# Kernel optimization log

Measured on AMD Instinct MI355X. Metric: run time of the kernel, lower is better.

The kernel has to match this reference:

```python
import jax, jax.numpy as jnp
import numpy as np

B = 16384
F_IN = 768
F_OUT = 512

def setup_inputs() -> dict:
    key = jax.random.key(0)
    k1, k2, k3, k4, k5, k6 = jax.random.split(key, 6)
    # densified sparse multi-hot boards (post to_dense())
    stm = jax.random.uniform(k1, (B, F_IN), dtype=jnp.float32)
    nstm = jax.random.uniform(k2, (B, F_IN), dtype=jnp.float32)
    s1 = 1.0 / np.sqrt(F_IN)
    s2 = 1.0 / np.sqrt(2 * F_OUT)
    W1 = jax.random.normal(k3, (F_OUT, F_IN), dtype=jnp.float32) * s1
    b1 = jax.random.normal(k4, (F_OUT,), dtype=jnp.float32) * s1
    W2 = jax.random.normal(k5, (1, 2 * F_OUT), dtype=jnp.float32) * s2
    b2 = jax.random.normal(k6, (1,), dtype=jnp.float32) * s2
    return {"stm": stm, "nstm": nstm, "W1": W1, "b1": b1, "W2": W2, "b2": b2}

def reference(stm, nstm, W1, b1, W2, b2):
    # shared feature transformer applied to both perspectives
    stm_p = stm @ W1.T + b1    # [B, F_OUT]
    nstm_p = nstm @ W1.T + b1  # [B, F_OUT]
    hidden = jnp.clip(jnp.concatenate((stm_p, nstm_p), axis=1), 0.0, 1.0)  # [B, 2*F_OUT]
    return jax.nn.sigmoid(hidden @ W2.T + b2)  # [B, 1]
```

## Files before the change

### kernel.cpp

```cpp
#include <hip/hip_runtime.h>
#include <hip/hip_bf16.h>

#define BATCH 16384
#define FIN   768
#define FOUT  512

#define BK 64
#define NT (FIN / BK)
#define BM 128
#define BN 256

typedef __attribute__((ext_vector_type(8))) short short8;
typedef __attribute__((ext_vector_type(4))) float floatx4;

__device__ __forceinline__ unsigned int cvt_pk_bf16(float a, float b) {
    unsigned int r;
    asm("v_cvt_pk_bf16_f32 %0, %1, %2" : "=v"(r) : "v"(a), "v"(b));
    return r;
}

__device__ __forceinline__ void load_lds_16(const void* g, void* l) {
    __builtin_amdgcn_global_load_lds(
        (const __attribute__((address_space(1))) unsigned int*)g,
        (__attribute__((address_space(3))) unsigned int*)l,
        16, 0, 0);
}

__global__ __launch_bounds__(256) void cvt_w1(
    const float* __restrict__ W1, unsigned short* __restrict__ W1b)
{
    int base = (blockIdx.x * 256 + threadIdx.x) * 8;
    float4 a = *(const float4*)(W1 + base);
    float4 b = *(const float4*)(W1 + base + 4);
    uint4 o;
    o.x = cvt_pk_bf16(a.x, a.y); o.y = cvt_pk_bf16(a.z, a.w);
    o.z = cvt_pk_bf16(b.x, b.y); o.w = cvt_pk_bf16(b.z, b.w);
    *(uint4*)(W1b + base) = o;
}

__global__ __launch_bounds__(512, 2) void pn_gemm(
    const float* __restrict__ stm, const float* __restrict__ nstm,
    const unsigned short* __restrict__ W1b, const float* __restrict__ b1,
    const float* __restrict__ W2, float* __restrict__ P)
{
    __shared__ __align__(16) unsigned short As[2][256 * 64];
    __shared__ __align__(16) unsigned short Bs[2][256 * 64];

    const int tid  = threadIdx.x;
    const int lane = tid & 63;
    const int wave = tid >> 6;
    const int wr   = wave >> 2;
    const int wc   = wave & 3;
    const int quad = lane >> 4;
    const int l16  = lane & 15;

    const int sbid  = (blockIdx.x & 7) * 32 + (blockIdx.x >> 3);
    const int bm    = sbid >> 1;
    const int n_idx = sbid & 1;
    const int b0    = bm * BM;
    const int n0    = n_idx * BN;

    const int arow = tid >> 1;
    const int h    = tid & 1;
    const float* aSrc =
        ((arow < BM) ? stm  + (size_t)(b0 + arow) * FIN
                     : nstm + (size_t)(b0 + arow - BM) * FIN) + h * 32;
    int aOff[4];
    #pragma unroll
    for (int c = 0; c < 4; ++c)
        aOff[c] = arow * 64 + (((h * 4 + c) ^ (arow & 7)) * 8);

    const int brow = lane >> 3;
    const int bch  = (lane & 7) ^ brow;
    const unsigned short* bSrc =
        W1b + (size_t)(n0 + brow) * FIN + bch * 8;

    floatx4 acc[8][4];
    #pragma unroll
    for (int i = 0; i < 8; ++i)
        #pragma unroll
        for (int j = 0; j < 4; ++j)
            acc[i][j] = (floatx4)0.0f;

    float4 ap[8];
    #pragma unroll
    for (int c = 0; c < 4; ++c) {
        ap[2 * c]     = *(const float4*)(aSrc + c * 8);
        ap[2 * c + 1] = *(const float4*)(aSrc + c * 8 + 4);
    }
    #pragma unroll
    for (int i = 0; i < 4; ++i) {
        const int J = wave * 4 + i;
        load_lds_16(bSrc + (size_t)(J * 8) * FIN, &Bs[0][J * 512]);
    }

    for (int t = 0; t < NT; ++t) {
        const int cur = t & 1;
        const int nxt = cur ^ 1;

        #pragma unroll
        for (int c = 0; c < 4; ++c) {
            uint4 o;
            o.x = cvt_pk_bf16(ap[2 * c].x, ap[2 * c].y);
            o.y = cvt_pk_bf16(ap[2 * c].z, ap[2 * c].w);
            o.z = cvt_pk_bf16(ap[2 * c + 1].x, ap[2 * c + 1].y);
            o.w = cvt_pk_bf16(ap[2 * c + 1].z, ap[2 * c + 1].w);
            *(uint4*)(&As[cur][aOff[c]]) = o;
        }
        __syncthreads();

        if (t + 1 < NT) {
            const int kn = (t + 1) * BK;
            #pragma unroll
            for (int c = 0; c < 4; ++c) {
                ap[2 * c]     = *(const float4*)(aSrc + kn + c * 8);
                ap[2 * c + 1] = *(const float4*)(aSrc + kn + c * 8 + 4);
            }
            #pragma unroll
            for (int i = 0; i < 4; ++i) {
                const int J = wave * 4 + i;
                load_lds_16(bSrc + (size_t)(J * 8) * FIN + kn, &Bs[nxt][J * 512]);
            }
        }

        #pragma unroll
        for (int kk = 0; kk < 2; ++kk) {
            const int c = kk * 4 + quad;
            short8 af[8], bfr[4];
            #pragma unroll
            for (int mi = 0; mi < 8; ++mi) {
                const int m = wr * 128 + mi * 16 + l16;
                af[mi] = *(const short8*)(&As[cur][m * 64 + ((c ^ (m & 7)) * 8)]);
            }
            #pragma unroll
            for (int ni = 0; ni < 4; ++ni) {
                const int n = wc * 64 + ni * 16 + l16;
                bfr[ni] = *(const short8*)(&Bs[cur][n * 64 + ((c ^ (n & 7)) * 8)]);
            }
            __builtin_amdgcn_s_setprio(1);
            #pragma unroll
            for (int mi = 0; mi < 8; ++mi)
                #pragma unroll
                for (int ni = 0; ni < 4; ++ni)
                    acc[mi][ni] = __builtin_amdgcn_mfma_f32_16x16x32_bf16(
                        af[mi], bfr[ni], acc[mi][ni], 0, 0, 0);
            __builtin_amdgcn_s_setprio(0);
        }
    }

    float b1v[4], w2v[4];
    const float* w2base = (wr == 0) ? W2 : W2 + FOUT;
    #pragma unroll
    for (int ni = 0; ni < 4; ++ni) {
        int col = n0 + wc * 64 + ni * 16 + l16;
        b1v[ni] = b1[col];
        w2v[ni] = w2base[col];
    }

    __syncthreads();
    float* Epi = (float*)As;

    #pragma unroll
    for (int mi = 0; mi < 8; ++mi) {
        #pragma unroll
        for (int r = 0; r < 4; ++r) {
            float s = 0.0f;
            #pragma unroll
            for (int ni = 0; ni < 4; ++ni) {
                float hh = acc[mi][ni][r] + b1v[ni];
                hh = fminf(fmaxf(hh, 0.0f), 1.0f);
                s += hh * w2v[ni];
            }
            s += __shfl_xor(s, 1);
            s += __shfl_xor(s, 2);
            s += __shfl_xor(s, 4);
            s += __shfl_xor(s, 8);
            if (l16 == 0) {
                Epi[(wr * 128 + mi * 16 + quad * 4 + r) * 4 + wc] = s;
            }
        }
    }
    __syncthreads();

    if (tid < BM) {
        float x = 0.0f;
        #pragma unroll
        for (int j = 0; j < 4; ++j)
            x += Epi[tid * 4 + j] + Epi[(tid + BM) * 4 + j];
        P[n_idx * BATCH + b0 + tid] = x;
    }
}

__global__ __launch_bounds__(256) void finish(
    const float* __restrict__ P, const float* __restrict__ b2,
    float* __restrict__ out)
{
    int i = blockIdx.x * 256 + threadIdx.x;
    float x = b2[0] + P[i] + P[BATCH + i];
    out[i] = 1.0f / (1.0f + expf(-x));
}

extern "C" void kernel_launch(void* const* d_in, const int* in_sizes, int n_in,
                              void* d_out, int out_size, void* d_ws, size_t ws_size,
                              hipStream_t stream)
{
    (void)in_sizes; (void)n_in; (void)out_size; (void)ws_size;
    const float* stm  = (const float*)d_in[0];
    const float* nstm = (const float*)d_in[1];
    const float* W1   = (const float*)d_in[2];
    const float* b1   = (const float*)d_in[3];
    const float* W2   = (const float*)d_in[4];
    const float* b2   = (const float*)d_in[5];
    float* out = (float*)d_out;
    unsigned short* W1b = (unsigned short*)d_ws;
    float* P = (float*)((char*)d_ws + FOUT * FIN * 2);

    cvt_w1<<<dim3((FOUT * FIN) / (256 * 8)), dim3(256), 0, stream>>>(W1, W1b);
    pn_gemm<<<dim3((BATCH / BM) * 2), dim3(512), 0, stream>>>(
        stm, nstm, W1b, b1, W2, P);
    finish<<<dim3(BATCH / 256), dim3(256), 0, stream>>>(P, b2, out);
}
```

Baseline: 163.7 us.

## Split GEMM k-step into four barrier-fenced MFMA phases with triple-buffered B

The main loop is restructured into four sub-phases, each handling half the M fragments and half the K chunk. Each phase is fenced by explicit s_barrier and sched_barrier so LDS fragment reads, the async global→LDS copies of W1 and the bf16 conversion of the next A tile are interleaved between MFMA bursts. B moves to a three-slot ring, prefetched two tiles ahead, and the A conversion and store for the next tile move to the end of the iteration. The goal is to hide global and LDS latency behind MFMA work. The cost is more barriers per tile and LDS growing to the full 160KB per block, and correctness depends on implicit vmcnt ordering for the async B loads.

```diff
diff --git a/kernel.cpp b/kernel.cpp
--- a/kernel.cpp
+++ b/kernel.cpp
@@ -25,6 +25,18 @@
         (__attribute__((address_space(3))) unsigned int*)l,
         16, 0, 0);
 }
+
+#define PH_OPEN() do {                                               \
+    __builtin_amdgcn_sched_barrier(0);                               \
+    __builtin_amdgcn_s_barrier();                                    \
+    asm volatile("s_waitcnt lgkmcnt(0)" ::: "memory");               \
+    __builtin_amdgcn_sched_barrier(0);                               \
+} while (0)
+#define PH_CLOSE() do {                                              \
+    __builtin_amdgcn_sched_barrier(0);                               \
+    __builtin_amdgcn_s_barrier();                                    \
+    __builtin_amdgcn_sched_barrier(0);                               \
+} while (0)
 
 __global__ __launch_bounds__(256) void cvt_w1(
     const float* __restrict__ W1, unsigned short* __restrict__ W1b)
@@ -44,7 +56,7 @@
     const float* __restrict__ W2, float* __restrict__ P)
 {
     __shared__ __align__(16) unsigned short As[2][256 * 64];
-    __shared__ __align__(16) unsigned short Bs[2][256 * 64];
+    __shared__ __align__(16) unsigned short Bs[3][256 * 64];
 
     const int tid  = threadIdx.x;
     const int lane = tid & 63;
@@ -82,6 +94,16 @@
         for (int j = 0; j < 4; ++j)
             acc[i][j] = (floatx4)0.0f;
 
+    #pragma unroll
+    for (int i = 0; i < 4; ++i) {
+        const int J = wave * 4 + i;
+        load_lds_16(bSrc + (size_t)(J * 8) * FIN, &Bs[0][J * 512]);
+    }
+    #pragma unroll
+    for (int i = 0; i < 4; ++i) {
+        const int J = wave * 4 + i;
+        load_lds_16(bSrc + (size_t)(J * 8) * FIN + BK, &Bs[1][J * 512]);
+    }
     float4 ap[8];
     #pragma unroll
     for (int c = 0; c < 4; ++c) {
@@ -89,25 +111,24 @@
         ap[2 * c + 1] = *(const float4*)(aSrc + c * 8 + 4);
     }
     #pragma unroll
-    for (int i = 0; i < 4; ++i) {
-        const int J = wave * 4 + i;
-        load_lds_16(bSrc + (size_t)(J * 8) * FIN, &Bs[0][J * 512]);
-    }
-
+    for (int c = 0; c < 4; ++c) {
+        uint4 o;
+        o.x = cvt_pk_bf16(ap[2 * c].x, ap[2 * c].y);
+        o.y = cvt_pk_bf16(ap[2 * c].z, ap[2 * c].w);
+        o.z = cvt_pk_bf16(ap[2 * c + 1].x, ap[2 * c + 1].y);
+        o.w = cvt_pk_bf16(ap[2 * c + 1].z, ap[2 * c + 1].w);
+        *(uint4*)(&As[0][aOff[c]]) = o;
+    }
+    __builtin_amdgcn_sched_barrier(0);
+    asm volatile("s_waitcnt lgkmcnt(0)" ::: "memory");
+    __builtin_amdgcn_s_barrier();
+    __builtin_amdgcn_sched_barrier(0);
+
+    int bc = 0;
     for (int t = 0; t < NT; ++t) {
         const int cur = t & 1;
-        const int nxt = cur ^ 1;
-
-        #pragma unroll
-        for (int c = 0; c < 4; ++c) {
-            uint4 o;
-            o.x = cvt_pk_bf16(ap[2 * c].x, ap[2 * c].y);
-            o.y = cvt_pk_bf16(ap[2 * c].z, ap[2 * c].w);
-            o.z = cvt_pk_bf16(ap[2 * c + 1].x, ap[2 * c + 1].y);
-            o.w = cvt_pk_bf16(ap[2 * c + 1].z, ap[2 * c + 1].w);
-            *(uint4*)(&As[cur][aOff[c]]) = o;
-        }
-        __syncthreads();
+        int bp = bc + 2; if (bp >= 3) bp -= 3;
+        short8 af[4], bf0[4], bf1[4];
 
         if (t + 1 < NT) {
             const int kn = (t + 1) * BK;
@@ -116,36 +137,122 @@
                 ap[2 * c]     = *(const float4*)(aSrc + kn + c * 8);
                 ap[2 * c + 1] = *(const float4*)(aSrc + kn + c * 8 + 4);
             }
-            #pragma unroll
-            for (int i = 0; i < 4; ++i) {
-                const int J = wave * 4 + i;
-                load_lds_16(bSrc + (size_t)(J * 8) * FIN + kn, &Bs[nxt][J * 512]);
-            }
-        }
-
-        #pragma unroll
-        for (int kk = 0; kk < 2; ++kk) {
-            const int c = kk * 4 + quad;
-            short8 af[8], bfr[4];
-            #pragma unroll
-            for (int mi = 0; mi < 8; ++mi) {
-                const int m = wr * 128 + mi * 16 + l16;
-                af[mi] = *(const short8*)(&As[cur][m * 64 + ((c ^ (m & 7)) * 8)]);
-            }
+        }
+        {
+            const int c0 = quad;
             #pragma unroll
             for (int ni = 0; ni < 4; ++ni) {
                 const int n = wc * 64 + ni * 16 + l16;
-                bfr[ni] = *(const short8*)(&Bs[cur][n * 64 + ((c ^ (n & 7)) * 8)]);
-            }
-            __builtin_amdgcn_s_setprio(1);
-            #pragma unroll
-            for (int mi = 0; mi < 8; ++mi)
-                #pragma unroll
-                for (int ni = 0; ni < 4; ++ni)
-                    acc[mi][ni] = __builtin_amdgcn_mfma_f32_16x16x32_bf16(
-                        af[mi], bfr[ni], acc[mi][ni], 0, 0, 0);
-            __builtin_amdgcn_s_setprio(0);
-        }
+                bf0[ni] = *(const short8*)(&Bs[bc][n * 64 + ((c0 ^ (n & 7)) * 8)]);
+            }
+            #pragma unroll
+            for (int mi = 0; mi < 4; ++mi) {
+                const int m = wr * 128 + mi * 16 + l16;
+                af[mi] = *(const short8*)(&As[cur][m * 64 + ((c0 ^ (m & 7)) * 8)]);
+            }
+        }
+        PH_OPEN();
+        __builtin_amdgcn_s_setprio(1);
+        #pragma unroll
+        for (int mi = 0; mi < 4; ++mi)
+            #pragma unroll
+            for (int ni = 0; ni < 4; ++ni)
+                acc[mi][ni] = __builtin_amdgcn_mfma_f32_16x16x32_bf16(
+                    af[mi], bf0[ni], acc[mi][ni], 0, 0, 0);
+        __builtin_amdgcn_s_setprio(0);
+        PH_CLOSE();
+
+        if (t + 2 < NT) {
+            const size_t kn2 = (size_t)(t + 2) * BK;
+            #pragma unroll
+            for (int i = 0; i < 2; ++i) {
+                const int J = wave * 4 + i;
+                load_lds_16(bSrc + (size_t)(J * 8) * FIN + kn2, &Bs[bp][J * 512]);
+            }
+        }
+        {
+            const int c0 = quad;
+            #pragma unroll
+            for (int mi = 0; mi < 4; ++mi) {
+                const int m = wr * 128 + (mi + 4) * 16 + l16;
+                af[mi] = *(const short8*)(&As[cur][m * 64 + ((c0 ^ (m & 7)) * 8)]);
+            }
+        }
+        PH_OPEN();
+        __builtin_amdgcn_s_setprio(1);
+        #pragma unroll
+        for (int mi = 0; mi < 4; ++mi)
+            #pragma unroll
+            for (int ni = 0; ni < 4; ++ni)
+                acc[mi + 4][ni] = __builtin_amdgcn_mfma_f32_16x16x32_bf16(
+                    af[mi], bf0[ni], acc[mi + 4][ni], 0, 0, 0);
+        __builtin_amdgcn_s_setprio(0);
+        PH_CLOSE();
+
+        if (t + 2 < NT) {
+            const size_t kn2 = (size_t)(t + 2) * BK;
+            #pragma unroll
+            for (int i = 2; i < 4; ++i) {
+                const int J = wave * 4 + i;
+                load_lds_16(bSrc + (size_t)(J * 8) * FIN + kn2, &Bs[bp][J * 512]);
+            }
+        }
+        {
+            const int c1 = 4 + quad;
+            #pragma unroll
+            for (int ni = 0; ni < 4; ++ni) {
+                const int n = wc * 64 + ni * 16 + l16;
+                bf1[ni] = *(const short8*)(&Bs[bc][n * 64 + ((c1 ^ (n & 7)) * 8)]);
+            }
+            #pragma unroll
+            for (int mi = 0; mi < 4; ++mi) {
+                const int m = wr * 128 + mi * 16 + l16;
+                af[mi] = *(const short8*)(&As[cur][m * 64 + ((c1 ^ (m & 7)) * 8)]);
+            }
+        }
+        PH_OPEN();
+        __builtin_amdgcn_s_setprio(1);
+        #pragma unroll
+        for (int mi = 0; mi < 4; ++mi)
+            #pragma unroll
+            for (int ni = 0; ni < 4; ++ni)
+                acc[mi][ni] = __builtin_amdgcn_mfma_f32_16x16x32_bf16(
+                    af[mi], bf1[ni], acc[mi][ni], 0, 0, 0);
+        __builtin_amdgcn_s_setprio(0);
+        PH_CLOSE();
+
+        if (t + 1 < NT) {
+            const int nxt = cur ^ 1;
+            #pragma unroll
+            for (int c = 0; c < 4; ++c) {
+                uint4 o;
+                o.x = cvt_pk_bf16(ap[2 * c].x, ap[2 * c].y);
+                o.y = cvt_pk_bf16(ap[2 * c].z, ap[2 * c].w);
+                o.z = cvt_pk_bf16(ap[2 * c + 1].x, ap[2 * c + 1].y);
+                o.w = cvt_pk_bf16(ap[2 * c + 1].z, ap[2 * c + 1].w);
+                *(uint4*)(&As[nxt][aOff[c]]) = o;
+            }
+        }
+        {
+            const int c1 = 4 + quad;
+            #pragma unroll
+            for (int mi = 0; mi < 4; ++mi) {
+                const int m = wr * 128 + (mi + 4) * 16 + l16;
+                af[mi] = *(const short8*)(&As[cur][m * 64 + ((c1 ^ (m & 7)) * 8)]);
+            }
+        }
+        PH_OPEN();
+        __builtin_amdgcn_s_setprio(1);
+        #pragma unroll
+        for (int mi = 0; mi < 4; ++mi)
+            #pragma unroll
+            for (int ni = 0; ni < 4; ++ni)
+                acc[mi + 4][ni] = __builtin_amdgcn_mfma_f32_16x16x32_bf16(
+                    af[mi], bf1[ni], acc[mi + 4][ni], 0, 0, 0);
+        __builtin_amdgcn_s_setprio(0);
+        PH_CLOSE();
+
+        bc = (bc == 2) ? 0 : bc + 1;
     }
 
     float b1v[4], w2v[4];
```

Measured after the change: 164.6 us. No clear change (+0.5%).
